# Kernel optimization log

Measured on AMD Instinct MI355X. Metric: run time of the kernel, lower is better.

The kernel has to match this reference:

```python
import jax, jax.numpy as jnp
import numpy as np

METRIC = [1, 1, 1, 1]  # Cl(4,0): 4 basis vectors squaring to +1 -> 16 blades


def _build_cayley(metric):
    """Dense geometric-product Cayley tensor C[i, j, k] for
    einsum('...i,ijk,...k->...j', a, C, b), blades in short-lex order
    (sorted by grade=popcount, then bitmap value)."""
    n = len(metric)
    N = 1 << n
    bitmaps = sorted(range(N), key=lambda bm: (bin(bm).count('1'), bm))
    bitmap_to_index = {bm: i for i, bm in enumerate(bitmaps)}
    cayley = np.zeros((N, N, N), dtype=np.float32)
    for i, ba in enumerate(bitmaps):
        for k, bb in enumerate(bitmaps):
            # reordering sign: count swaps to merge basis-vector lists
            a_sh = ba >> 1
            swaps = 0
            while a_sh:
                swaps += bin(a_sh & bb).count('1')
                a_sh >>= 1
            sign = -1.0 if (swaps & 1) else 1.0
            # contracted common basis vectors pick up metric factors
            common = ba & bb
            for m in range(n):
                if common & (1 << m):
                    sign *= float(metric[m])
            j = bitmap_to_index[ba ^ bb]
            cayley[i, j, k] = sign
    return jnp.asarray(cayley)


def setup_inputs() -> dict:
    key = jax.random.key(0)
    k1, k2 = jax.random.split(key)
    B, T, NB = 2048, 1024, 1 << len(METRIC)  # NB = 16 blades
    a = jax.random.normal(k1, (B, T, NB), dtype=jnp.float32)
    b = jax.random.normal(k2, (B, T, NB), dtype=jnp.float32)
    cayley = _build_cayley(METRIC)  # [16, 16, 16] structured sign table (buffer)
    return {"a": a, "b": b, "cayley": cayley}


def reference(a, b, cayley):
    # CliffordAlgebra.geometric_product(a, b):
    #   torch.einsum('...i,ijk,...k->...j', a, cayley, b)
    return jnp.einsum('...i,ijk,...k->...j', a, cayley, b)
```

## Files before the change

kernel.cpp:

```cpp
#include <hip/hip_runtime.h>

struct Tables {
    signed char  sgn[16][16];
    unsigned char out[16][16];
};

constexpr int pc4(int x) {
    return ((x >> 0) & 1) + ((x >> 1) & 1) + ((x >> 2) & 1) + ((x >> 3) & 1);
}

constexpr Tables make_tables() {
    Tables t{};
    int bitmaps[16] = {};
    int n = 0;
    for (int g = 0; g <= 4; ++g)
        for (int bm = 0; bm < 16; ++bm)
            if (pc4(bm) == g) bitmaps[n++] = bm;
    int inv[16] = {};
    for (int i = 0; i < 16; ++i) inv[bitmaps[i]] = i;
    for (int i = 0; i < 16; ++i) {
        for (int k = 0; k < 16; ++k) {
            const int ba = bitmaps[i];
            const int bb = bitmaps[k];
            int swaps = 0;
            for (int sh = ba >> 1; sh; sh >>= 1) swaps += pc4(sh & bb);
            t.sgn[i][k] = (swaps & 1) ? -1 : 1;
            t.out[i][k] = (unsigned char)inv[ba ^ bb];
        }
    }
    return t;
}

constexpr Tables TBL = make_tables();

__global__ __launch_bounds__(256) void clifford_gp_kernel(
        const float4* __restrict__ a4,
        const float4* __restrict__ b4,
        float4* __restrict__ o4,
        int n_mv) {
    const int m = blockIdx.x * blockDim.x + threadIdx.x;
    if (m >= n_mv) return;

    float av[16], bv[16], ov[16];

    #pragma unroll
    for (int q = 0; q < 4; ++q) {
        const float4 va = a4[m * 4 + q];
        av[q * 4 + 0] = va.x; av[q * 4 + 1] = va.y;
        av[q * 4 + 2] = va.z; av[q * 4 + 3] = va.w;
    }
    #pragma unroll
    for (int q = 0; q < 4; ++q) {
        const float4 vb = b4[m * 4 + q];
        bv[q * 4 + 0] = vb.x; bv[q * 4 + 1] = vb.y;
        bv[q * 4 + 2] = vb.z; bv[q * 4 + 3] = vb.w;
    }

    #pragma unroll
    for (int j = 0; j < 16; ++j) ov[j] = 0.0f;

    #pragma unroll
    for (int i = 0; i < 16; ++i) {
        #pragma unroll
        for (int k = 0; k < 16; ++k) {
            const int j = TBL.out[i][k];
            if (TBL.sgn[i][k] > 0) {
                ov[j] = fmaf(av[i], bv[k], ov[j]);
            } else {
                ov[j] = fmaf(-av[i], bv[k], ov[j]);
            }
        }
    }

    #pragma unroll
    for (int q = 0; q < 4; ++q) {
        o4[m * 4 + q] = make_float4(ov[q * 4 + 0], ov[q * 4 + 1],
                                    ov[q * 4 + 2], ov[q * 4 + 3]);
    }
}

extern "C" void kernel_launch(void* const* d_in, const int* in_sizes, int n_in,
                              void* d_out, int out_size, void* d_ws, size_t ws_size,
                              hipStream_t stream) {
    const float4* a4 = (const float4*)d_in[0];
    const float4* b4 = (const float4*)d_in[1];
    float4* o4 = (float4*)d_out;

    const int n_mv = in_sizes[0] / 16;
    const int block = 256;
    const int grid = (n_mv + block - 1) / block;

    clifford_gp_kernel<<<grid, block, 0, stream>>>(a4, b4, o4, n_mv);
}
```

Baseline: 310.2 us.

## Stage inputs and outputs through padded LDS for coalesced global access

Adjacent threads now load consecutive float4s from global memory into padded shared memory, then each thread reads its own 16-float multivector from LDS. The output goes back the same way, through LDS and then as coalesced float4 stores. This replaces the old 64-byte-strided per-thread float4 accesses, which may coalesce poorly. In exchange it adds about 34KB of LDS per block, two barriers and scalar LDS traffic, which could lower occupancy.

```diff
diff --git a/kernel.cpp b/kernel.cpp
--- a/kernel.cpp
+++ b/kernel.cpp
@@ -33,28 +33,41 @@
 
 constexpr Tables TBL = make_tables();
 
+#define ROW 17
+
 __global__ __launch_bounds__(256) void clifford_gp_kernel(
         const float4* __restrict__ a4,
         const float4* __restrict__ b4,
         float4* __restrict__ o4,
         int n_mv) {
-    const int m = blockIdx.x * blockDim.x + threadIdx.x;
-    if (m >= n_mv) return;
+    __shared__ float lds_a[256 * ROW];
+    __shared__ float lds_b[256 * ROW];
+
+    const int t = threadIdx.x;
+    const int base4 = blockIdx.x * 256 * 4;
+    const int n4 = n_mv * 4;
+
+    #pragma unroll
+    for (int r = 0; r < 4; ++r) {
+        const int idx = r * 256 + t;
+        if (base4 + idx < n4) {
+            const float4 va = a4[base4 + idx];
+            const float4 vb = b4[base4 + idx];
+            const int mv = idx >> 2;
+            const int q  = idx & 3;
+            float* pa = &lds_a[mv * ROW + q * 4];
+            pa[0] = va.x; pa[1] = va.y; pa[2] = va.z; pa[3] = va.w;
+            float* pb = &lds_b[mv * ROW + q * 4];
+            pb[0] = vb.x; pb[1] = vb.y; pb[2] = vb.z; pb[3] = vb.w;
+        }
+    }
+    __syncthreads();
 
     float av[16], bv[16], ov[16];
-
     #pragma unroll
-    for (int q = 0; q < 4; ++q) {
-        const float4 va = a4[m * 4 + q];
-        av[q * 4 + 0] = va.x; av[q * 4 + 1] = va.y;
-        av[q * 4 + 2] = va.z; av[q * 4 + 3] = va.w;
-    }
+    for (int c = 0; c < 16; ++c) av[c] = lds_a[t * ROW + c];
     #pragma unroll
-    for (int q = 0; q < 4; ++q) {
-        const float4 vb = b4[m * 4 + q];
-        bv[q * 4 + 0] = vb.x; bv[q * 4 + 1] = vb.y;
-        bv[q * 4 + 2] = vb.z; bv[q * 4 + 3] = vb.w;
-    }
+    for (int c = 0; c < 16; ++c) bv[c] = lds_b[t * ROW + c];
 
     #pragma unroll
     for (int j = 0; j < 16; ++j) ov[j] = 0.0f;
@@ -73,9 +86,18 @@
     }
 
     #pragma unroll
-    for (int q = 0; q < 4; ++q) {
-        o4[m * 4 + q] = make_float4(ov[q * 4 + 0], ov[q * 4 + 1],
-                                    ov[q * 4 + 2], ov[q * 4 + 3]);
+    for (int c = 0; c < 16; ++c) lds_a[t * ROW + c] = ov[c];
+    __syncthreads();
+
+    #pragma unroll
+    for (int r = 0; r < 4; ++r) {
+        const int idx = r * 256 + t;
+        if (base4 + idx < n4) {
+            const int mv = idx >> 2;
+            const int q  = idx & 3;
+            const float* po = &lds_a[mv * ROW + q * 4];
+            o4[base4 + idx] = make_float4(po[0], po[1], po[2], po[3]);
+        }
     }
 }
 
```

Result: no change. 311.1 us (+0.3%).
